# Kernel tuning notes

Hardware: AMD Instinct MI355X
Metric: run time of the kernel (lower is better)

The kernel has to match this reference:

```python
import jax, jax.numpy as jnp
import numpy as np

T, IN, OUT = 16384, 4096, 4096


def setup_inputs() -> dict:
    key = jax.random.key(0)
    k1, k2, k3, k4, k5 = jax.random.split(key, 5)
    x = jax.random.randint(k1, (T, IN), -128, 128, dtype=jnp.int32)      # int8-valued activations
    weight = jax.random.randint(k2, (OUT, IN), -128, 128, dtype=jnp.int32)  # int8-valued weights
    bias = jax.random.randint(k3, (OUT,), -128, 128, dtype=jnp.int32)    # int8-valued bias
    # requant scales: alpha = a_scale*w_scale/o_scale, beta = b_scale/o_scale
    alpha = jax.random.uniform(k4, (1,), jnp.float32, 1e-4, 1e-3)
    beta = jax.random.uniform(k5, (1,), jnp.float32, 0.5, 1.5)
    return {"x": x, "weight": weight, "bias": bias, "alpha": alpha, "beta": beta}


def reference(x, weight, bias, alpha, beta):
    # INT8 GEMM with int32 accumulation: acc[t,o] = sum_i x[t,i] * W[o,i]
    acc = jnp.einsum('ti,oi->to', x, weight,
                     preferred_element_type=jnp.int32)  # [T, OUT] int32
    # inline dequant + bias + requant epilogue
    y = acc.astype(jnp.float32) * alpha + bias.astype(jnp.float32) * beta
    # round and saturate to int8 output (W8A8B8O8)
    out = jnp.clip(jnp.round(y), -128.0, 127.0).astype(jnp.int8)
    return out
```

## Files before the change

kernel.cpp:

```cpp
#include <hip/hip_runtime.h>
#include <stdint.h>

constexpr int T_DIM   = 16384;
constexpr int IN_DIM  = 4096;
constexpr int OUT_DIM = 4096;

using int32x4 = __attribute__((ext_vector_type(4))) int;

#define GLOAD_LDS16(g, l)                                                     \
    __builtin_amdgcn_global_load_lds(                                         \
        (const __attribute__((address_space(1))) void*)(uintptr_t)(g),        \
        (__attribute__((address_space(3))) void*)(uintptr_t)(l), 16, 0, 0)

__global__ void pack_swz(const int* __restrict__ src, int8_t* __restrict__ dst,
                         int rows, int cols) {
    int64_t tid = (int64_t)blockIdx.x * blockDim.x + threadIdx.x;
    int64_t nchunks = (int64_t)rows * (cols / 16);
    if (tid >= nchunks) return;
    int row  = (int)(tid / (cols / 16));
    int cidx = (int)(tid % (cols / 16));
    const int32x4* s4 =
        reinterpret_cast<const int32x4*>(src + (int64_t)row * cols + (cidx << 4));
    uint32_t p[4];
#pragma unroll
    for (int v = 0; v < 4; ++v) {
        int32x4 t = s4[v];
        p[v] = (uint32_t)(t[0] & 0xff) | ((uint32_t)(t[1] & 0xff) << 8) |
               ((uint32_t)(t[2] & 0xff) << 16) | ((uint32_t)(t[3] & 0xff) << 24);
    }
    int cs = (cidx & ~3) | ((cidx & 3) ^ ((row >> 1) & 3));
    *reinterpret_cast<int32x4*>(dst + (int64_t)row * cols + (cs << 4)) =
        *reinterpret_cast<int32x4*>(p);
}

constexpr int BM = 256, BN = 256, BK = 64;
constexpr int NT    = IN_DIM / BK;
constexpr int ATILE = BM * BK;
constexpr int BUFSZ = 2 * ATILE;

__global__ __launch_bounds__(512, 2)
void gemm_i8_8p(const int8_t* __restrict__ x8, const int8_t* __restrict__ w8,
                const int* __restrict__ bias, const float* __restrict__ alphap,
                const float* __restrict__ betap, int* __restrict__ out) {
    __shared__ __align__(16) int8_t lds[4 * BUFSZ];

    const int tid  = threadIdx.x;
    const int lane = tid & 63;
    const int wid  = tid >> 6;
    const int wr   = wid >> 2;
    const int wc   = wid & 3;

    const int nwg = gridDim.x;
    const int cpx = nwg >> 3;
    const int bid = blockIdx.x;
    const int swz = (bid & 7) * cpx + (bid >> 3);
    const int bm  = swz >> 4;
    const int bn  = swz & 15;
    const int brow = bm * BM;
    const int bcol = bn * BN;

    const float alpha = *alphap;
    const float beta  = *betap;

    const int g = lane >> 4;
    const int r = lane & 15;

    const int offL0 = tid * 16;
    const int offL1 = 8192 + tid * 16;
    const int rowL0 = offL0 >> 6, inL0 = offL0 & 63;
    const int rowL1 = offL1 >> 6, inL1 = offL1 & 63;
    const int8_t* pA0 = x8 + (int64_t)(brow + rowL0) * IN_DIM + inL0;
    const int8_t* pA1 = x8 + (int64_t)(brow + rowL1) * IN_DIM + inL1;
    const int8_t* pB0 = w8 + (int64_t)(bcol + rowL0) * IN_DIM + inL0;
    const int8_t* pB1 = w8 + (int64_t)(bcol + rowL1) * IN_DIM + inL1;
    const int dA0 = offL0, dA1 = offL1;
    const int dB0 = ATILE + offL0, dB1 = ATILE + offL1;

    int aoff[8], boff[4];
#pragma unroll
    for (int m = 0; m < 8; ++m) {
        const int row = wr * 128 + m * 16 + r;
        aoff[m] = row * BK + ((g ^ ((row >> 1) & 3)) << 4);
    }
#pragma unroll
    for (int n = 0; n < 4; ++n) {
        const int row = wc * 64 + n * 16 + r;
        boff[n] = ATILE + row * BK + ((g ^ ((row >> 1) & 3)) << 4);
    }

    int32x4 acc[8][4] = {};

#define KTILE(BIDX, PF, VM)                                                    \
    do {                                                                       \
        const int8_t* buf = lds + (BIDX) * BUFSZ;                              \
        int8_t* nxt = lds + (((BIDX) + 3) & 3) * BUFSZ;                        \
        if (PF) {                                                              \
            GLOAD_LDS16(pA0, nxt + dA0);  GLOAD_LDS16(pA1, nxt + dA1);         \
            GLOAD_LDS16(pB0, nxt + dB0);  GLOAD_LDS16(pB1, nxt + dB1);         \
            pA0 += BK; pA1 += BK; pB0 += BK; pB1 += BK;                        \
        }                                                                      \
        int32x4 af[8], bf[4];                                                  \
        _Pragma("unroll") for (int n = 0; n < 4; ++n)                          \
            bf[n] = *reinterpret_cast<const int32x4*>(buf + boff[n]);          \
        _Pragma("unroll") for (int m = 0; m < 8; ++m)                          \
            af[m] = *reinterpret_cast<const int32x4*>(buf + aoff[m]);          \
        __builtin_amdgcn_s_setprio(1);                                         \
        _Pragma("unroll") for (int m = 0; m < 8; ++m)                          \
            _Pragma("unroll") for (int n = 0; n < 4; ++n)                      \
                acc[m][n] = __builtin_amdgcn_mfma_i32_16x16x64_i8(             \
                    af[m], bf[n], acc[m][n], 0, 0, 0);                         \
        __builtin_amdgcn_s_setprio(0);                                         \
        if ((VM) == 8)      asm volatile("s_waitcnt vmcnt(8)" ::: "memory");   \
        else if ((VM) == 4) asm volatile("s_waitcnt vmcnt(4)" ::: "memory");   \
        else if ((VM) == 0) asm volatile("s_waitcnt vmcnt(0)" ::: "memory");   \
        __builtin_amdgcn_s_barrier();                                          \
        asm volatile("" ::: "memory");       \
    } while (0)

#pragma unroll
    for (int t = 0; t < 3; ++t) {
        int8_t* buf = lds + t * BUFSZ;
        GLOAD_LDS16(pA0, buf + dA0);  GLOAD_LDS16(pA1, buf + dA1);
        GLOAD_LDS16(pB0, buf + dB0);  GLOAD_LDS16(pB1, buf + dB1);
        pA0 += BK; pA1 += BK; pB0 += BK; pB1 += BK;
    }
    asm volatile("s_waitcnt vmcnt(8)" ::: "memory");
    __builtin_amdgcn_s_barrier();
    asm volatile("" ::: "memory");

#pragma unroll 1
    for (int tt = 0; tt < NT - 4; tt += 4) {
        KTILE(0, true, 8);
        KTILE(1, true, 8);
        KTILE(2, true, 8);
        KTILE(3, true, 8);
    }
    KTILE(0, true,  8);
    KTILE(1, false, 4);
    KTILE(2, false, 0);
    KTILE(3, false, -1);
#undef KTILE

    const int r4 = (lane >> 4) * 4;
    const int cl = lane & 15;
#pragma unroll
    for (int n = 0; n < 4; ++n) {
        const int col = bcol + wc * 64 + n * 16 + cl;
        const float bterm = (float)bias[col] * beta;
#pragma unroll
        for (int m = 0; m < 8; ++m) {
            const int row0 = brow + wr * 128 + m * 16 + r4;
#pragma unroll
            for (int j = 0; j < 4; ++j) {
                float y = (float)acc[m][n][j] * alpha + bterm;
                y = rintf(y);
                y = fminf(fmaxf(y, -128.0f), 127.0f);
                out[(int64_t)(row0 + j) * OUT_DIM + col] = (int)y;
            }
        }
    }
}

__global__ __launch_bounds__(256)
void gemm_i8_fb(const int* __restrict__ x32, const int* __restrict__ w32,
                const int* __restrict__ bias, const float* __restrict__ alphap,
                const float* __restrict__ betap, int* __restrict__ out) {
    constexpr int FBM = 128, FBK = 128;
    __shared__ int8_t lA[FBM * FBK];
    __shared__ int8_t lB[FBM * FBK];

    const int tid  = threadIdx.x;
    const int wid  = tid >> 6;
    const int lane = tid & 63;
    const int nwg = gridDim.x;
    const int cpx = nwg >> 3;
    const int bid = blockIdx.x;
    const int swz = (bid & 7) * cpx + (bid >> 3);
    const int brow = (swz >> 5) * FBM;
    const int bcol = (swz & 31) * FBM;
    const int wr = wid >> 1, wc = wid & 1;
    const float alpha = *alphap;
    const float beta  = *betap;

    int32x4 acc[4][4] = {};
    for (int kt = 0; kt < IN_DIM / FBK; ++kt) {
        const int64_t kbase = (int64_t)kt * FBK;
#pragma unroll
        for (int q = 0; q < 4; ++q) {
            const int off = wid * 4096 + q * 1024 + lane * 16;
            const int row = off >> 7;
            const int k   = off & 127;
            const int* ga = x32 + (int64_t)(brow + row) * IN_DIM + kbase + k;
            const int* gb = w32 + (int64_t)(bcol + row) * IN_DIM + kbase + k;
            uint32_t pa[4], pb[4];
#pragma unroll
            for (int v = 0; v < 4; ++v) {
                int32x4 ta = reinterpret_cast<const int32x4*>(ga)[v];
                int32x4 tb = reinterpret_cast<const int32x4*>(gb)[v];
                pa[v] = (uint32_t)(ta[0] & 0xff) | ((uint32_t)(ta[1] & 0xff) << 8) |
                        ((uint32_t)(ta[2] & 0xff) << 16) | ((uint32_t)(ta[3] & 0xff) << 24);
                pb[v] = (uint32_t)(tb[0] & 0xff) | ((uint32_t)(tb[1] & 0xff) << 8) |
                        ((uint32_t)(tb[2] & 0xff) << 16) | ((uint32_t)(tb[3] & 0xff) << 24);
            }
            const int sc = ((k >> 4) ^ (row & 7)) << 4;
            *reinterpret_cast<int32x4*>(lA + row * FBK + sc) = *reinterpret_cast<int32x4*>(pa);
            *reinterpret_cast<int32x4*>(lB + row * FBK + sc) = *reinterpret_cast<int32x4*>(pb);
        }
        __syncthreads();
#pragma unroll
        for (int ks = 0; ks < 2; ++ks) {
            const int gg = lane >> 4, rr = lane & 15;
            const int lc = ks * 4 + gg;
            int32x4 af[4], bf[4];
#pragma unroll
            for (int m = 0; m < 4; ++m) {
                const int row = wr * 64 + m * 16 + rr;
                af[m] = *reinterpret_cast<const int32x4*>(lA + row * FBK + ((lc ^ (row & 7)) << 4));
            }
#pragma unroll
            for (int n = 0; n < 4; ++n) {
                const int row = wc * 64 + n * 16 + rr;
                bf[n] = *reinterpret_cast<const int32x4*>(lB + row * FBK + ((lc ^ (row & 7)) << 4));
            }
#pragma unroll
            for (int m = 0; m < 4; ++m)
#pragma unroll
                for (int n = 0; n < 4; ++n)
                    acc[m][n] = __builtin_amdgcn_mfma_i32_16x16x64_i8(af[m], bf[n], acc[m][n], 0, 0, 0);
        }
        __syncthreads();
    }
    const int r4 = (lane >> 4) * 4;
    const int cl = lane & 15;
#pragma unroll
    for (int n = 0; n < 4; ++n) {
        const int col = bcol + wc * 64 + n * 16 + cl;
        const float bterm = (float)bias[col] * beta;
#pragma unroll
        for (int m = 0; m < 4; ++m) {
            const int row0 = brow + wr * 64 + m * 16 + r4;
#pragma unroll
            for (int j = 0; j < 4; ++j) {
                float y = (float)acc[m][n][j] * alpha + bterm;
                y = rintf(y);
                y = fminf(fmaxf(y, -128.0f), 127.0f);
                out[(int64_t)(row0 + j) * OUT_DIM + col] = (int)y;
            }
        }
    }
}

extern "C" void kernel_launch(void* const* d_in, const int* in_sizes, int n_in,
                              void* d_out, int out_size, void* d_ws, size_t ws_size,
                              hipStream_t stream) {
    const int*   x     = (const int*)d_in[0];
    const int*   w     = (const int*)d_in[1];
    const int*   bias  = (const int*)d_in[2];
    const float* alpha = (const float*)d_in[3];
    const float* beta  = (const float*)d_in[4];
    int*         out   = (int*)d_out;

    const size_t need = (size_t)T_DIM * IN_DIM + (size_t)OUT_DIM * IN_DIM;

    if (ws_size >= need) {
        int8_t* x8 = (int8_t*)d_ws;
        int8_t* w8 = x8 + (size_t)T_DIM * IN_DIM;
        {
            int64_t nch = (int64_t)T_DIM * (IN_DIM / 16);
            pack_swz<<<(int)((nch + 255) / 256), 256, 0, stream>>>(x, x8, T_DIM, IN_DIM);
        }
        {
            int64_t nch = (int64_t)OUT_DIM * (IN_DIM / 16);
            pack_swz<<<(int)((nch + 255) / 256), 256, 0, stream>>>(w, w8, OUT_DIM, IN_DIM);
        }
        const int grid = (T_DIM / BM) * (OUT_DIM / BN);
        gemm_i8_8p<<<grid, 512, 0, stream>>>(x8, w8, bias, alpha, beta, out);
    } else {
        const int grid = (T_DIM / 128) * (OUT_DIM / 128);
        gemm_i8_fb<<<grid, 256, 0, stream>>>(x, w, bias, alpha, beta, out);
    }
}
```

Baseline: 394.6 us.

## Double-buffer LDS-to-register fragments to overlap reads with MFMA

Restructures the main K loop so the LDS fragments for the next tile are read into a second register set while the MFMAs for the current tile run from the first set, ping-ponging between them. The global-to-LDS prefetch distance and the vmcnt waits are adjusted to match (prefetch depth changes from 3 ahead to effectively 2 ahead with vmcnt(4)). This aims to hide LDS read latency behind matrix math, at the cost of doubled fragment registers (extra 48 VGPRs) and a shallower global prefetch.

```diff
diff --git a/kernel.cpp b/kernel.cpp
--- a/kernel.cpp
+++ b/kernel.cpp
@@ -89,57 +89,67 @@
     }
 
     int32x4 acc[8][4] = {};
-
-#define KTILE(BIDX, PF, VM)                                                    \
+    int32x4 fA0[8], fB0[4], fA1[8], fB1[4];
+
+#define STAGE4(BIDX)                                                           \
     do {                                                                       \
-        const int8_t* buf = lds + (BIDX) * BUFSZ;                              \
-        int8_t* nxt = lds + (((BIDX) + 3) & 3) * BUFSZ;                        \
-        if (PF) {                                                              \
-            GLOAD_LDS16(pA0, nxt + dA0);  GLOAD_LDS16(pA1, nxt + dA1);         \
-            GLOAD_LDS16(pB0, nxt + dB0);  GLOAD_LDS16(pB1, nxt + dB1);         \
-            pA0 += BK; pA1 += BK; pB0 += BK; pB1 += BK;                        \
-        }                                                                      \
-        int32x4 af[8], bf[4];                                                  \
+        int8_t* nb = lds + (BIDX) * BUFSZ;                                     \
+        GLOAD_LDS16(pA0, nb + dA0);  GLOAD_LDS16(pA1, nb + dA1);               \
+        GLOAD_LDS16(pB0, nb + dB0);  GLOAD_LDS16(pB1, nb + dB1);               \
+        pA0 += BK; pA1 += BK; pB0 += BK; pB1 += BK;                            \
+    } while (0)
+
+#define TILE(READB, STAGEB, FAC, FBC, FAN, FBN, PF, VM)                        \
+    do {                                                                       \
+        if (PF) STAGE4(STAGEB);                                                \
+        const int8_t* rb = lds + (READB) * BUFSZ;                              \
         _Pragma("unroll") for (int n = 0; n < 4; ++n)                          \
-            bf[n] = *reinterpret_cast<const int32x4*>(buf + boff[n]);          \
+            FBN[n] = *reinterpret_cast<const int32x4*>(rb + boff[n]);          \
         _Pragma("unroll") for (int m = 0; m < 8; ++m)                          \
-            af[m] = *reinterpret_cast<const int32x4*>(buf + aoff[m]);          \
+            FAN[m] = *reinterpret_cast<const int32x4*>(rb + aoff[m]);          \
         __builtin_amdgcn_s_setprio(1);                                         \
         _Pragma("unroll") for (int m = 0; m < 8; ++m)                          \
             _Pragma("unroll") for (int n = 0; n < 4; ++n)                      \
                 acc[m][n] = __builtin_amdgcn_mfma_i32_16x16x64_i8(             \
-                    af[m], bf[n], acc[m][n], 0, 0, 0);                         \
+                    FAC[m], FBC[n], acc[m][n], 0, 0, 0);                       \
         __builtin_amdgcn_s_setprio(0);                                         \
-        if ((VM) == 8)      asm volatile("s_waitcnt vmcnt(8)" ::: "memory");   \
-        else if ((VM) == 4) asm volatile("s_waitcnt vmcnt(4)" ::: "memory");   \
+        if ((VM) == 4)      asm volatile("s_waitcnt vmcnt(4)" ::: "memory");   \
         else if ((VM) == 0) asm volatile("s_waitcnt vmcnt(0)" ::: "memory");   \
         __builtin_amdgcn_s_barrier();                                          \
-        asm volatile("" ::: "memory");       \
+        asm volatile("" ::: "memory");                                         \
     } while (0)
 
-#pragma unroll
-    for (int t = 0; t < 3; ++t) {
-        int8_t* buf = lds + t * BUFSZ;
-        GLOAD_LDS16(pA0, buf + dA0);  GLOAD_LDS16(pA1, buf + dA1);
-        GLOAD_LDS16(pB0, buf + dB0);  GLOAD_LDS16(pB1, buf + dB1);
-        pA0 += BK; pA1 += BK; pB0 += BK; pB1 += BK;
-    }
-    asm volatile("s_waitcnt vmcnt(8)" ::: "memory");
+    STAGE4(0); STAGE4(1); STAGE4(2);
+    asm volatile("s_waitcnt vmcnt(4)" ::: "memory");
     __builtin_amdgcn_s_barrier();
     asm volatile("" ::: "memory");
+#pragma unroll
+    for (int n = 0; n < 4; ++n)
+        fB0[n] = *reinterpret_cast<const int32x4*>(lds + boff[n]);
+#pragma unroll
+    for (int m = 0; m < 8; ++m)
+        fA0[m] = *reinterpret_cast<const int32x4*>(lds + aoff[m]);
 
 #pragma unroll 1
     for (int tt = 0; tt < NT - 4; tt += 4) {
-        KTILE(0, true, 8);
-        KTILE(1, true, 8);
-        KTILE(2, true, 8);
-        KTILE(3, true, 8);
-    }
-    KTILE(0, true,  8);
-    KTILE(1, false, 4);
-    KTILE(2, false, 0);
-    KTILE(3, false, -1);
-#undef KTILE
+        TILE(1, 3, fA0, fB0, fA1, fB1, true, 4);
+        TILE(2, 0, fA1, fB1, fA0, fB0, true, 4);
+        TILE(3, 1, fA0, fB0, fA1, fB1, true, 4);
+        TILE(0, 2, fA1, fB1, fA0, fB0, true, 4);
+    }
+    TILE(1, 3, fA0, fB0, fA1, fB1, true,  4);
+    TILE(2, 0, fA1, fB1, fA0, fB0, false, 0);
+    TILE(3, 0, fA0, fB0, fA1, fB1, false, -1);
+    __builtin_amdgcn_s_setprio(1);
+#pragma unroll
+    for (int m = 0; m < 8; ++m)
+#pragma unroll
+        for (int n = 0; n < 4; ++n)
+            acc[m][n] = __builtin_amdgcn_mfma_i32_16x16x64_i8(
+                fA1[m], fB1[n], acc[m][n], 0, 0, 0);
+    __builtin_amdgcn_s_setprio(0);
+#undef TILE
+#undef STAGE4
 
     const int r4 = (lane >> 4) * 4;
     const int cl = lane & 15;
```

New measurement: 540.7 us. 1.37x slower.
